# Kernel tuning notes

Measured on AMD Instinct MI355X. Metric: run time of the kernel, lower is better.

## Reference

```python
import jax, jax.numpy as jnp
import numpy as np

N_EMBED = 1024
NUM_EXPERTS = 8
TOP_K = 2
N_ROUTERS = 5
SEQ = 2048


def setup_inputs() -> dict:
    key = jax.random.key(0)
    ks = jax.random.split(key, 10)
    d, E, R, H = N_EMBED, NUM_EXPERTS, N_ROUTERS, 4 * N_EMBED
    x = jax.random.normal(ks[0], (R, SEQ, d), dtype=jnp.float32)
    moe = jnp.arange(R, dtype=jnp.int64) if jax.config.jax_enable_x64 else jnp.arange(R, dtype=jnp.int32)
    s = 0.02
    Wr = s * jax.random.normal(ks[1], (R, d, E), dtype=jnp.float32)
    br = jnp.zeros((R, E), dtype=jnp.float32)
    Wn = s * jax.random.normal(ks[2], (R, d, E), dtype=jnp.float32)
    bn = jnp.zeros((R, E), dtype=jnp.float32)
    W1 = s * jax.random.normal(ks[3], (E, d, H), dtype=jnp.float32)
    b1 = jnp.zeros((E, H), dtype=jnp.float32)
    W2 = s * jax.random.normal(ks[4], (E, H, d), dtype=jnp.float32)
    b2 = jnp.zeros((E, d), dtype=jnp.float32)
    return {"x": x, "moe": moe, "Wr": Wr, "br": br, "Wn": Wn, "bn": bn,
            "W1": W1, "b1": b1, "W2": W2, "b2": b2}


def reference(x, moe, Wr, br, Wn, bn, W1, b1, W2, b2):
    # Per-batch router selection: router[moe[b]] applied to x[b]
    logits = jnp.einsum('btd,bde->bte', x, Wr[moe]) + br[moe][:, None, :]
    noise_logits = jnp.einsum('btd,bde->bte', x, Wn[moe]) + bn[moe][:, None, :]
    eps = jax.random.normal(jax.random.key(42), logits.shape, logits.dtype)
    noisy = logits + eps * jax.nn.softplus(noise_logits)  # [B,T,E]

    topv, topi = jax.lax.top_k(noisy, TOP_K)  # [B,T,K]
    E = noisy.shape[-1]
    # selected[b,t,e] = e in top-k indices; equivalent to scatter of top-k logits into -inf
    selected = jnp.any(topi[..., None] == jnp.arange(E), axis=-2)  # [B,T,E]
    sparse = jnp.where(selected, noisy, -jnp.inf)
    gating = jax.nn.softmax(sparse, axis=-1)  # zero for non-selected experts

    B, T, d = x.shape
    flat_x = x.reshape(-1, d)            # [B*T, d]
    flat_g = gating.reshape(-1, E)       # [B*T, E]
    out = jnp.zeros_like(flat_x)
    for e in range(E):  # fixed small set of experts
        h = jax.nn.relu(flat_x @ W1[e] + b1[e])   # [B*T, 4d]
        o = h @ W2[e] + b2[e]                      # [B*T, d]
        out = out + o * flat_g[:, e:e + 1]         # gating is 0 off top-k
    final_output = out.reshape(B, T, d)
    return final_output, topi
```

## Files before the change

### kernel.cpp

```cpp
#include <hip/hip_runtime.h>
#include <hip/hip_bf16.h>
#include <cstdint>

#define NTOK   10240
#define DIM    1024
#define NEXP   8
#define HDIM   4096
#define NSLOT  20480
#define MAXSLOT 21504
#define MAXTILES 168

typedef __attribute__((ext_vector_type(8))) __bf16 bf16x8;
typedef __attribute__((ext_vector_type(4))) float  f32x4;

__device__ __forceinline__ unsigned short f2bf(float f){
  uint32_t u = __float_as_uint(f);
  uint32_t r = (u + 0x7fffu + ((u >> 16) & 1u)) >> 16;
  return (unsigned short)r;
}
__device__ __forceinline__ float bf2f(unsigned short u){
  return __uint_as_float(((uint32_t)u) << 16);
}

__device__ __forceinline__ void gl_lds16(const void* g, void* l){
  __builtin_amdgcn_global_load_lds(
      (const __attribute__((address_space(1))) void*)g,
      (__attribute__((address_space(3))) void*)l, 16, 0, 0);
}

__device__ __forceinline__ int swz_wid(){
  int nwg = (int)(gridDim.x * gridDim.y);
  int h   = (int)(blockIdx.y * gridDim.x + blockIdx.x);
  int q = nwg >> 3, r = nwg & 7;
  int xcd = h & 7, idx = h >> 3;
  return (xcd < r ? xcd*(q+1) : r*(q+1) + (xcd-r)*q) + idx;
}

__device__ __forceinline__ uint32_t rotl32(uint32_t x, int n){ return (x << n) | (x >> (32 - n)); }

__device__ __forceinline__ uint32_t threefry_xor(uint32_t k0, uint32_t k1, uint32_t x0, uint32_t x1){
  uint32_t ks2 = k0 ^ k1 ^ 0x1BD11BDAu;
  uint32_t ks[3] = {k0, k1, ks2};
  x0 += ks[0]; x1 += ks[1];
  const int rA[4] = {13,15,26,6};
  const int rB[4] = {17,29,16,24};
  #pragma unroll
  for (int i = 0; i < 5; ++i){
    #pragma unroll
    for (int j = 0; j < 4; ++j){
      int rot = (i & 1) ? rB[j] : rA[j];
      x0 += x1; x1 = rotl32(x1, rot); x1 ^= x0;
    }
    x0 += ks[(i+1)%3];
    x1 += ks[(i+2)%3] + (uint32_t)(i+1);
  }
  return x0 ^ x1;
}

__device__ __forceinline__ float erfinv_f32(float x){
  float w = -log1pf(-x*x);
  float p;
  if (w < 5.0f){
    w -= 2.5f;
    p = 2.81022636e-08f;
    p = fmaf(p, w, 3.43273939e-07f);
    p = fmaf(p, w, -3.5233877e-06f);
    p = fmaf(p, w, -4.39150654e-06f);
    p = fmaf(p, w, 0.00021858087f);
    p = fmaf(p, w, -0.00125372503f);
    p = fmaf(p, w, -0.00417768164f);
    p = fmaf(p, w, 0.246640727f);
    p = fmaf(p, w, 1.50140941f);
  } else {
    w = sqrtf(w) - 3.0f;
    p = -0.000200214257f;
    p = fmaf(p, w, 0.000100950558f);
    p = fmaf(p, w, 0.00134934322f);
    p = fmaf(p, w, -0.00367342844f);
    p = fmaf(p, w, 0.00573950773f);
    p = fmaf(p, w, -0.0076224613f);
    p = fmaf(p, w, 0.00943887047f);
    p = fmaf(p, w, 1.00167406f);
    p = fmaf(p, w, 2.83297682f);
  }
  return p * x;
}

__global__ void transpose_cvt_kernel(const float* __restrict__ src, unsigned short* __restrict__ dst,
                                     int R_, int C_){
  __shared__ float tile[32][33];
  int z = blockIdx.z;
  const float* s = src + (size_t)z * R_ * C_;
  unsigned short* d = dst + (size_t)z * R_ * C_;
  int c0 = blockIdx.x * 32, r0 = blockIdx.y * 32;
  #pragma unroll
  for (int i = threadIdx.y; i < 32; i += 8)
    tile[i][threadIdx.x] = s[(size_t)(r0 + i) * C_ + c0 + threadIdx.x];
  __syncthreads();
  #pragma unroll
  for (int i = threadIdx.y; i < 32; i += 8)
    d[(size_t)(c0 + i) * R_ + r0 + threadIdx.x] = f2bf(tile[threadIdx.x][i]);
}

__global__ __launch_bounds__(256) void route_kernel(
    const float* __restrict__ x, const int* __restrict__ moe,
    const float* __restrict__ Wr, const float* __restrict__ br,
    const float* __restrict__ Wn, const float* __restrict__ bn,
    float* __restrict__ topi_out, int* __restrict__ te, float* __restrict__ tgv,
    unsigned short* __restrict__ xb)
{
  const int wv = threadIdx.x >> 6, lane = threadIdx.x & 63;
  const int tok = (int)blockIdx.x * 4 + wv;
  const int b = tok >> 11;
  const int r = moe[b];
  const float4* xr  = (const float4*)(x + (size_t)tok * DIM);
  const float4* wrp = (const float4*)(Wr + (size_t)r * DIM * NEXP);
  const float4* wnp = (const float4*)(Wn + (size_t)r * DIM * NEXP);
  ushort4* xbrow = (ushort4*)(xb + (size_t)tok * DIM);

  float lg[8], nl[8];
  #pragma unroll
  for (int e = 0; e < 8; ++e){ lg[e] = 0.f; nl[e] = 0.f; }

  #pragma unroll
  for (int it = 0; it < 4; ++it){
    int d4 = it*64 + lane;
    float4 xv = xr[d4];
    ushort4 o;
    o.x = f2bf(xv.x); o.y = f2bf(xv.y); o.z = f2bf(xv.z); o.w = f2bf(xv.w);
    xbrow[d4] = o;
    #pragma unroll
    for (int j = 0; j < 4; ++j){
      float xs = (j==0) ? xv.x : (j==1) ? xv.y : (j==2) ? xv.z : xv.w;
      float4 w0 = wrp[d4*8 + j*2], w1 = wrp[d4*8 + j*2 + 1];
      float4 n0 = wnp[d4*8 + j*2], n1 = wnp[d4*8 + j*2 + 1];
      lg[0] = fmaf(xs, w0.x, lg[0]); lg[1] = fmaf(xs, w0.y, lg[1]);
      lg[2] = fmaf(xs, w0.z, lg[2]); lg[3] = fmaf(xs, w0.w, lg[3]);
      lg[4] = fmaf(xs, w1.x, lg[4]); lg[5] = fmaf(xs, w1.y, lg[5]);
      lg[6] = fmaf(xs, w1.z, lg[6]); lg[7] = fmaf(xs, w1.w, lg[7]);
      nl[0] = fmaf(xs, n0.x, nl[0]); nl[1] = fmaf(xs, n0.y, nl[1]);
      nl[2] = fmaf(xs, n0.z, nl[2]); nl[3] = fmaf(xs, n0.w, nl[3]);
      nl[4] = fmaf(xs, n1.x, nl[4]); nl[5] = fmaf(xs, n1.y, nl[5]);
      nl[6] = fmaf(xs, n1.z, nl[6]); nl[7] = fmaf(xs, n1.w, nl[7]);
    }
  }

  #pragma unroll
  for (int e = 0; e < 8; ++e){
    #pragma unroll
    for (int s = 32; s >= 1; s >>= 1){
      lg[e] += __shfl_xor(lg[e], s, 64);
      nl[e] += __shfl_xor(nl[e], s, 64);
    }
  }

  int el = lane & 7;
  float mylg = lg[0], mynl = nl[0];
  #pragma unroll
  for (int e = 1; e < 8; ++e){
    if (el == e){ mylg = lg[e]; mynl = nl[e]; }
  }
  float logit = mylg + br[r*NEXP + el];
  float nlg   = mynl + bn[r*NEXP + el];
  uint32_t idx  = (uint32_t)(tok*NEXP + el);
  uint32_t bits = threefry_xor(0u, 42u, 0u, idx);
  float u01 = __uint_as_float((bits >> 9) | 0x3f800000u) - 1.0f;
  const float lo = -0.99999994f;
  float uu  = fmaxf(lo, u01 * 2.0f + lo);
  float eps = 1.41421356237f * erfinv_f32(uu);
  float ax = fabsf(nlg);
  float sp = fmaxf(nlg, 0.0f) + log1pf(expf(-ax));
  float noisy = logit + eps * sp;

  float nv[8];
  #pragma unroll
  for (int e = 0; e < 8; ++e) nv[e] = __shfl(noisy, e, 64);

  if (lane == 0){
    int i0 = 0; float v0 = nv[0];
    int i1 = -1; float v1 = -3.4e38f;
    #pragma unroll
    for (int e = 1; e < 8; ++e){
      float v = nv[e];
      if (v > v0){ v1 = v0; i1 = i0; v0 = v; i0 = e; }
      else if (v > v1){ v1 = v; i1 = e; }
    }
    float t = expf(v1 - v0);
    float s = 1.0f + t;
    topi_out[tok*2 + 0] = (float)i0;
    topi_out[tok*2 + 1] = (float)i1;
    te[tok*2 + 0] = i0; te[tok*2 + 1] = i1;
    tgv[tok*2 + 0] = 1.0f / s; tgv[tok*2 + 1] = t / s;
  }
}

__global__ __launch_bounds__(256) void count_kernel(const int* __restrict__ te,
                                                    unsigned* __restrict__ counts){
  int id = blockIdx.x * 256 + threadIdx.x;
  int e = te[id];
  int lane = threadIdx.x & 63;
  #pragma unroll
  for (int ee = 0; ee < 8; ++ee){
    unsigned long long m = __ballot(e == ee);
    if (m && lane == (__ffsll((unsigned long long)m) - 1))
      atomicAdd(&counts[ee], (unsigned)__popcll(m));
  }
}

__global__ void tables_kernel(unsigned* __restrict__ hdr, int* __restrict__ tile_expert,
                              int* __restrict__ rows)
{
  __shared__ unsigned offs_s[NEXP+1];
  __shared__ unsigned cnt_s[NEXP];
  if (threadIdx.x == 0){
    unsigned o = 0, tt = 0;
    for (int e = 0; e < NEXP; ++e){
      unsigned c = hdr[e];
      cnt_s[e] = c;
      offs_s[e] = o;
      hdr[8 + e] = o;
      unsigned nt = (c + 127u) / 128u;
      for (unsigned k = 0; k < nt; ++k) tile_expert[tt++] = e;
      o += nt * 128u;
    }
    offs_s[NEXP] = o;
    hdr[16] = tt;
  }
  __syncthreads();
  for (int e = 0; e < NEXP; ++e){
    unsigned start = offs_s[e] + cnt_s[e];
    unsigned end   = offs_s[e+1];
    for (unsigned i = start + threadIdx.x; i < end; i += blockDim.x)
      rows[i] = 0;
  }
}

__global__ __launch_bounds__(256) void scatter_kernel(const int* __restrict__ te,
                               unsigned* __restrict__ cursor, int* __restrict__ rows,
                               int* __restrict__ slot_idx)
{
  int id = blockIdx.x * 256 + threadIdx.x;
  int tok = id >> 1;
  int e = te[id];
  int lane = threadIdx.x & 63;
  unsigned long long below = ((unsigned long long)1 << lane) - 1ull;
  unsigned myslot = 0;
  #pragma unroll
  for (int ee = 0; ee < 8; ++ee){
    unsigned long long m = __ballot(e == ee);
    if (e == ee){
      int leader = __ffsll((unsigned long long)m) - 1;
      unsigned base = 0;
      if (lane == leader) base = atomicAdd(&cursor[ee], (unsigned)__popcll(m));
      base = __shfl(base, leader, 64);
      myslot = base + (unsigned)__popcll(m & below);
    }
  }
  rows[myslot] = tok;
  slot_idx[id] = (int)myslot;
}

__global__ __launch_bounds__(512) void gemm1_kernel(
    const unsigned short* __restrict__ Xb,
    const unsigned short* __restrict__ W1t,
    const float* __restrict__ b1,
    const int* __restrict__ rows, const int* __restrict__ tile_expert,
    const unsigned* __restrict__ hdr,
    unsigned short* __restrict__ H)
{
  const int w  = swz_wid();
  const int xn = w % (int)gridDim.x;
  const int tg = w / (int)gridDim.x;
  if (tg >= (int)hdr[16]) return;
  const int e  = tile_expert[tg];
  const int n0 = xn * 128;
  const int tid = threadIdx.x;
  const int wid = tid >> 6, lane = tid & 63;
  const int wr = wid >> 2, wc = wid & 3;
  const int l8 = lane & 7, ld8 = lane >> 3;
  const int srcsw = (l8 ^ ld8) * 8;
  const int l15 = lane & 15, lq = lane >> 4, l7 = lane & 7;

  __shared__ __align__(16) unsigned short As[2][128][64];
  __shared__ __align__(16) unsigned short Bs[2][128][64];

  const unsigned short* aSrc[2];
  const unsigned short* bSrc[2];
  #pragma unroll
  for (int i = 0; i < 2; ++i){
    int rrow = wid*16 + i*8 + ld8;
    int tokr = rows[tg*128 + rrow];
    aSrc[i] = Xb  + (size_t)tokr * DIM + srcsw;
    bSrc[i] = W1t + ((size_t)e * HDIM + n0 + rrow) * DIM + srcsw;
  }

  f32x4 acc[4][2];
  #pragma unroll
  for (int m = 0; m < 4; ++m)
    #pragma unroll
    for (int n = 0; n < 2; ++n) acc[m][n] = (f32x4)(0.0f);

  auto stage = [&](int b, int kk){
    #pragma unroll
    for (int i = 0; i < 2; ++i){
      gl_lds16(aSrc[i] + kk, &As[b][wid*16 + i*8][0]);
      gl_lds16(bSrc[i] + kk, &Bs[b][wid*16 + i*8][0]);
    }
  };

  stage(0, 0);
  __builtin_amdgcn_sched_barrier(0);

  const int NT = DIM / 64;
  int cur = 0;
  for (int t = 0; t < NT; ++t){
    if (t + 1 < NT){
      stage(cur ^ 1, (t + 1) * 64);
      __builtin_amdgcn_sched_barrier(0);
      asm volatile("s_waitcnt vmcnt(4)" ::: "memory");
    } else {
      asm volatile("s_waitcnt vmcnt(0)" ::: "memory");
    }
    __builtin_amdgcn_sched_barrier(0);
    __builtin_amdgcn_s_barrier();
    __builtin_amdgcn_sched_barrier(0);

    #pragma unroll
    for (int ks = 0; ks < 2; ++ks){
      const int ch = ((ks*4 + lq) ^ l7) * 8;
      bf16x8 af[4], bfv[2];
      #pragma unroll
      for (int m = 0; m < 4; ++m)
        af[m] = *reinterpret_cast<const bf16x8*>(&As[cur][wr*64 + m*16 + l15][ch]);
      #pragma unroll
      for (int n = 0; n < 2; ++n)
        bfv[n] = *reinterpret_cast<const bf16x8*>(&Bs[cur][wc*32 + n*16 + l15][ch]);
      __builtin_amdgcn_s_setprio(1);
      #pragma unroll
      for (int m = 0; m < 4; ++m)
        #pragma unroll
        for (int n = 0; n < 2; ++n)
          acc[m][n] = __builtin_amdgcn_mfma_f32_16x16x32_bf16(af[m], bfv[n], acc[m][n], 0, 0, 0);
      __builtin_amdgcn_s_setprio(0);
    }
    __builtin_amdgcn_sched_barrier(0);
    __builtin_amdgcn_s_barrier();
    __builtin_amdgcn_sched_barrier(0);
    cur ^= 1;
  }

  const int hrow0 = tg * 128;
  #pragma unroll
  for (int n = 0; n < 2; ++n){
    int c = n0 + wc*32 + n*16 + l15;
    float bv = b1[(size_t)e * HDIM + c];
    #pragma unroll
    for (int m = 0; m < 4; ++m){
      #pragma unroll
      for (int j = 0; j < 4; ++j){
        int rloc = wr*64 + m*16 + lq*4 + j;
        float v = fmaxf(acc[m][n][j] + bv, 0.0f);
        H[(size_t)(hrow0 + rloc) * HDIM + c] = f2bf(v);
      }
    }
  }
}

__global__ __launch_bounds__(512) void gemm2_kernel(
    const unsigned short* __restrict__ H,
    const unsigned short* __restrict__ W2t,
    const float* __restrict__ b2,
    const int* __restrict__ tile_expert, const unsigned* __restrict__ hdr,
    unsigned short* __restrict__ O2)
{
  const int w  = swz_wid();
  const int xn = w % (int)gridDim.x;
  const int tg = w / (int)gridDim.x;
  if (tg >= (int)hdr[16]) return;
  const int e  = tile_expert[tg];
  const int n0 = xn * 128;
  const int tid = threadIdx.x;
  const int wid = tid >> 6, lane = tid & 63;
  const int wr = wid >> 2, wc = wid & 3;
  const int l8 = lane & 7, ld8 = lane >> 3;
  const int srcsw = (l8 ^ ld8) * 8;
  const int l15 = lane & 15, lq = lane >> 4, l7 = lane & 7;

  __shared__ __align__(16) unsigned short As[2][128][64];
  __shared__ __align__(16) unsigned short Bs[2][128][64];

  const unsigned short* aSrc[2];
  const unsigned short* bSrc[2];
  #pragma unroll
  for (int i = 0; i < 2; ++i){
    int rrow = wid*16 + i*8 + ld8;
    aSrc[i] = H   + (size_t)(tg*128 + rrow) * HDIM + srcsw;
    bSrc[i] = W2t + ((size_t)e * DIM + n0 + rrow) * HDIM + srcsw;
  }

  f32x4 acc[4][2];
  #pragma unroll
  for (int m = 0; m < 4; ++m)
    #pragma unroll
    for (int n = 0; n < 2; ++n) acc[m][n] = (f32x4)(0.0f);

  auto stage = [&](int b, int kk){
    #pragma unroll
    for (int i = 0; i < 2; ++i){
      gl_lds16(aSrc[i] + kk, &As[b][wid*16 + i*8][0]);
      gl_lds16(bSrc[i] + kk, &Bs[b][wid*16 + i*8][0]);
    }
  };

  stage(0, 0);
  __builtin_amdgcn_sched_barrier(0);

  const int NT = HDIM / 64;
  int cur = 0;
  for (int t = 0; t < NT; ++t){
    if (t + 1 < NT){
      stage(cur ^ 1, (t + 1) * 64);
      __builtin_amdgcn_sched_barrier(0);
      asm volatile("s_waitcnt vmcnt(4)" ::: "memory");
    } else {
      asm volatile("s_waitcnt vmcnt(0)" ::: "memory");
    }
    __builtin_amdgcn_sched_barrier(0);
    __builtin_amdgcn_s_barrier();
    __builtin_amdgcn_sched_barrier(0);

    #pragma unroll
    for (int ks = 0; ks < 2; ++ks){
      const int ch = ((ks*4 + lq) ^ l7) * 8;
      bf16x8 af[4], bfv[2];
      #pragma unroll
      for (int m = 0; m < 4; ++m)
        af[m] = *reinterpret_cast<const bf16x8*>(&As[cur][wr*64 + m*16 + l15][ch]);
      #pragma unroll
      for (int n = 0; n < 2; ++n)
        bfv[n] = *reinterpret_cast<const bf16x8*>(&Bs[cur][wc*32 + n*16 + l15][ch]);
      __builtin_amdgcn_s_setprio(1);
      #pragma unroll
      for (int m = 0; m < 4; ++m)
        #pragma unroll
        for (int n = 0; n < 2; ++n)
          acc[m][n] = __builtin_amdgcn_mfma_f32_16x16x32_bf16(af[m], bfv[n], acc[m][n], 0, 0, 0);
      __builtin_amdgcn_s_setprio(0);
    }
    __builtin_amdgcn_sched_barrier(0);
    __builtin_amdgcn_s_barrier();
    __builtin_amdgcn_sched_barrier(0);
    cur ^= 1;
  }

  #pragma unroll
  for (int n = 0; n < 2; ++n){
    int c = n0 + wc*32 + n*16 + l15;
    float bv = b2[(size_t)e * DIM + c];
    #pragma unroll
    for (int m = 0; m < 4; ++m){
      #pragma unroll
      for (int j = 0; j < 4; ++j){
        int rloc = wr*64 + m*16 + lq*4 + j;
        O2[(size_t)(tg*128 + rloc) * DIM + c] = f2bf(acc[m][n][j] + bv);
      }
    }
  }
}

__global__ __launch_bounds__(256) void combine_kernel(
    const unsigned short* __restrict__ O2, const int* __restrict__ slot_idx,
    const float* __restrict__ tgv, float* __restrict__ out)
{
  int tok = blockIdx.x;
  int d4  = threadIdx.x;
  int s0 = slot_idx[tok*2], s1 = slot_idx[tok*2 + 1];
  float g0 = tgv[tok*2], g1 = tgv[tok*2 + 1];
  ushort4 a = ((const ushort4*)(O2 + (size_t)s0 * DIM))[d4];
  ushort4 b = ((const ushort4*)(O2 + (size_t)s1 * DIM))[d4];
  float4 o;
  o.x = g0*bf2f(a.x) + g1*bf2f(b.x);
  o.y = g0*bf2f(a.y) + g1*bf2f(b.y);
  o.z = g0*bf2f(a.z) + g1*bf2f(b.z);
  o.w = g0*bf2f(a.w) + g1*bf2f(b.w);
  ((float4*)(out + (size_t)tok * DIM))[d4] = o;
}

extern "C" void kernel_launch(void* const* d_in, const int* in_sizes, int n_in,
                              void* d_out, int out_size, void* d_ws, size_t ws_size,
                              hipStream_t stream)
{
  const float* x  = (const float*)d_in[0];
  const int*   moe= (const int*)  d_in[1];
  const float* Wr = (const float*)d_in[2];
  const float* br = (const float*)d_in[3];
  const float* Wn = (const float*)d_in[4];
  const float* bn = (const float*)d_in[5];
  const float* W1 = (const float*)d_in[6];
  const float* b1 = (const float*)d_in[7];
  const float* W2 = (const float*)d_in[8];
  const float* b2 = (const float*)d_in[9];
  float* out = (float*)d_out;
  float* topi_out = out + (size_t)NTOK * DIM;

  char* ws = (char*)d_ws;
  size_t off = 0;
  auto take = [&](size_t bytes)->char*{
    char* p = ws + off;
    off = (off + bytes + 255) & ~(size_t)255;
    return p;
  };
  unsigned* hdr        = (unsigned*)take(128);
  int*      tile_exp   = (int*)     take(MAXTILES * 4);
  int*      rows       = (int*)     take(MAXSLOT * 4);
  int*      te         = (int*)     take(NSLOT * 4);
  float*    tgv        = (float*)   take(NSLOT * 4);
  int*      slot_idx   = (int*)     take(NSLOT * 4);
  unsigned short* xb   = (unsigned short*)take((size_t)NTOK * DIM * 2);
  unsigned short* W1t  = (unsigned short*)take((size_t)NEXP * HDIM * DIM * 2);
  unsigned short* W2t  = (unsigned short*)take((size_t)NEXP * DIM * HDIM * 2);
  unsigned short* O2   = (unsigned short*)take((size_t)MAXSLOT * DIM * 2);

  size_t avail = (ws_size > off) ? (ws_size - off) : 0;
  size_t maxrows = avail / ((size_t)HDIM * 2);
  int tpc = (int)(maxrows / 128);
  if (tpc > MAXTILES) tpc = MAXTILES;
  if (tpc < 1) tpc = 1;
  unsigned short* H = (unsigned short*)take((size_t)tpc * 128 * HDIM * 2);

  hipMemsetAsync(hdr, 0, 128, stream);

  dim3 tb(32, 8);
  transpose_cvt_kernel<<<dim3(HDIM/32, DIM/32, NEXP), tb, 0, stream>>>(W1, W1t, DIM, HDIM);
  transpose_cvt_kernel<<<dim3(DIM/32, HDIM/32, NEXP), tb, 0, stream>>>(W2, W2t, HDIM, DIM);
  route_kernel<<<NTOK/4, 256, 0, stream>>>(x, moe, Wr, br, Wn, bn, topi_out, te, tgv, xb);
  count_kernel<<<NSLOT/256, 256, 0, stream>>>(te, hdr);
  tables_kernel<<<1, 64, 0, stream>>>(hdr, tile_exp, rows);
  scatter_kernel<<<NSLOT/256, 256, 0, stream>>>(te, hdr + 8, rows, slot_idx);

  if (tpc >= MAXTILES){
    gemm1_kernel<<<dim3(HDIM/128, MAXTILES), 512, 0, stream>>>(xb, W1t, b1, rows, tile_exp, hdr, H);
    gemm2_kernel<<<dim3(DIM/128,  MAXTILES), 512, 0, stream>>>(H, W2t, b2, tile_exp, hdr, O2);
  } else {
    for (int t0 = 0; t0 < MAXTILES; t0 += tpc){
      int nt = (tpc < MAXTILES - t0) ? tpc : (MAXTILES - t0);
      unsigned short* Hoff = H - (size_t)t0 * 128 * HDIM;
      gemm1_kernel<<<dim3(HDIM/128, nt), 512, 0, stream>>>(xb, W1t, b1, rows + t0*128,
                                                           tile_exp + t0, hdr, Hoff);
      gemm2_kernel<<<dim3(DIM/128,  nt), 512, 0, stream>>>(Hoff, W2t, b2, tile_exp + t0, hdr,
                                                           O2 + (size_t)t0*128*DIM);
    }
  }
  combine_kernel<<<NTOK, 256, 0, stream>>>(O2, slot_idx, tgv, out);
}
```

Before: 735.5 us.

## Merge weight transposes into routing kernel and deepen GEMM prefetch pipeline

Folds the two weight transpose/convert launches into the routing kernel as extra blocks, saving launches and letting the transposes overlap with routing. Both expert GEMMs switch from a 2-stage pipeline over 64-wide K slices to a 4-slot pipeline over 32-wide half-tiles with three stages in flight, which hides more global-load latency. The XOR swizzle on LDS is dropped in favour of a plain 32-column layout. That may add LDS bank conflicts, and it doubles the barriers per unit of K.

```diff
diff --git a/kernel.cpp b/kernel.cpp
--- a/kernel.cpp
+++ b/kernel.cpp
@@ -86,33 +86,49 @@
   return p * x;
 }
 
-__global__ void transpose_cvt_kernel(const float* __restrict__ src, unsigned short* __restrict__ dst,
-                                     int R_, int C_){
+__device__ __forceinline__ void transpose_body(const float* __restrict__ src,
+                                               unsigned short* __restrict__ dst,
+                                               int R_, int C_, int bx, int by, int z){
   __shared__ float tile[32][33];
-  int z = blockIdx.z;
+  const int tx = threadIdx.x & 31, ty = threadIdx.x >> 5;
   const float* s = src + (size_t)z * R_ * C_;
   unsigned short* d = dst + (size_t)z * R_ * C_;
-  int c0 = blockIdx.x * 32, r0 = blockIdx.y * 32;
-  #pragma unroll
-  for (int i = threadIdx.y; i < 32; i += 8)
-    tile[i][threadIdx.x] = s[(size_t)(r0 + i) * C_ + c0 + threadIdx.x];
+  int c0 = bx * 32, r0 = by * 32;
+  #pragma unroll
+  for (int i = ty; i < 32; i += 8)
+    tile[i][tx] = s[(size_t)(r0 + i) * C_ + c0 + tx];
   __syncthreads();
   #pragma unroll
-  for (int i = threadIdx.y; i < 32; i += 8)
-    d[(size_t)(c0 + i) * R_ + r0 + threadIdx.x] = f2bf(tile[threadIdx.x][i]);
-}
-
-__global__ __launch_bounds__(256) void route_kernel(
+  for (int i = ty; i < 32; i += 8)
+    d[(size_t)(c0 + i) * R_ + r0 + tx] = f2bf(tile[tx][i]);
+}
+
+__global__ __launch_bounds__(256) void prep_kernel(
     const float* __restrict__ x, const int* __restrict__ moe,
     const float* __restrict__ Wr, const float* __restrict__ br,
     const float* __restrict__ Wn, const float* __restrict__ bn,
+    const float* __restrict__ W1, const float* __restrict__ W2,
     float* __restrict__ topi_out, int* __restrict__ te, float* __restrict__ tgv,
-    unsigned short* __restrict__ xb)
-{
+    unsigned short* __restrict__ xb,
+    unsigned short* __restrict__ W1t, unsigned short* __restrict__ W2t)
+{
+  const int b = (int)blockIdx.x;
+  const int NROUTE = NTOK/4;
+  if (b >= NROUTE){
+    int i = b - NROUTE;
+    if (i < 32768){
+      transpose_body(W1, W1t, DIM, HDIM, i & 127, (i >> 7) & 31, i >> 12);
+    } else {
+      i -= 32768;
+      transpose_body(W2, W2t, HDIM, DIM, i & 31, (i >> 5) & 127, i >> 12);
+    }
+    return;
+  }
+
   const int wv = threadIdx.x >> 6, lane = threadIdx.x & 63;
-  const int tok = (int)blockIdx.x * 4 + wv;
-  const int b = tok >> 11;
-  const int r = moe[b];
+  const int tok = b * 4 + wv;
+  const int bb = tok >> 11;
+  const int r = moe[bb];
   const float4* xr  = (const float4*)(x + (size_t)tok * DIM);
   const float4* wrp = (const float4*)(Wr + (size_t)r * DIM * NEXP);
   const float4* wnp = (const float4*)(Wn + (size_t)r * DIM * NEXP);
@@ -277,22 +293,16 @@
   const int tid = threadIdx.x;
   const int wid = tid >> 6, lane = tid & 63;
   const int wr = wid >> 2, wc = wid & 3;
-  const int l8 = lane & 7, ld8 = lane >> 3;
-  const int srcsw = (l8 ^ ld8) * 8;
-  const int l15 = lane & 15, lq = lane >> 4, l7 = lane & 7;
-
-  __shared__ __align__(16) unsigned short As[2][128][64];
-  __shared__ __align__(16) unsigned short Bs[2][128][64];
-
-  const unsigned short* aSrc[2];
-  const unsigned short* bSrc[2];
-  #pragma unroll
-  for (int i = 0; i < 2; ++i){
-    int rrow = wid*16 + i*8 + ld8;
-    int tokr = rows[tg*128 + rrow];
-    aSrc[i] = Xb  + (size_t)tokr * DIM + srcsw;
-    bSrc[i] = W1t + ((size_t)e * HDIM + n0 + rrow) * DIM + srcsw;
-  }
+  const int l15 = lane & 15, lq = lane >> 4;
+  const int srow = wid*16 + (lane >> 2);
+  const int sch  = lane & 3;
+
+  __shared__ __align__(16) unsigned short As[2][2][128][32];
+  __shared__ __align__(16) unsigned short Bs[2][2][128][32];
+
+  const int tokr = rows[tg*128 + srow];
+  const unsigned short* aRow = Xb  + (size_t)tokr * DIM + sch*8;
+  const unsigned short* bRow = W1t + ((size_t)e * HDIM + n0 + srow) * DIM + sch*8;
 
   f32x4 acc[4][2];
   #pragma unroll
@@ -300,53 +310,45 @@
     #pragma unroll
     for (int n = 0; n < 2; ++n) acc[m][n] = (f32x4)(0.0f);
 
-  auto stage = [&](int b, int kk){
-    #pragma unroll
-    for (int i = 0; i < 2; ++i){
-      gl_lds16(aSrc[i] + kk, &As[b][wid*16 + i*8][0]);
-      gl_lds16(bSrc[i] + kk, &Bs[b][wid*16 + i*8][0]);
-    }
+  auto stage = [&](int h){
+    gl_lds16(aRow + h*32, &As[(h>>1)&1][h&1][wid*16][0]);
+    gl_lds16(bRow + h*32, &Bs[(h>>1)&1][h&1][wid*16][0]);
   };
 
-  stage(0, 0);
+  const int HT = DIM / 32;
+  stage(0); stage(1); stage(2);
   __builtin_amdgcn_sched_barrier(0);
 
-  const int NT = DIM / 64;
-  int cur = 0;
-  for (int t = 0; t < NT; ++t){
-    if (t + 1 < NT){
-      stage(cur ^ 1, (t + 1) * 64);
-      __builtin_amdgcn_sched_barrier(0);
-      asm volatile("s_waitcnt vmcnt(4)" ::: "memory");
-    } else {
-      asm volatile("s_waitcnt vmcnt(0)" ::: "memory");
-    }
+  for (int h = 0; h < HT; ++h){
+    if (h + 3 < HT) stage(h + 3);
+    __builtin_amdgcn_sched_barrier(0);
+    int rem = HT - 1 - h;
+    if (rem >= 3)      asm volatile("s_waitcnt vmcnt(6)" ::: "memory");
+    else if (rem == 2) asm volatile("s_waitcnt vmcnt(4)" ::: "memory");
+    else if (rem == 1) asm volatile("s_waitcnt vmcnt(2)" ::: "memory");
+    else               asm volatile("s_waitcnt vmcnt(0)" ::: "memory");
     __builtin_amdgcn_sched_barrier(0);
     __builtin_amdgcn_s_barrier();
     __builtin_amdgcn_sched_barrier(0);
 
-    #pragma unroll
-    for (int ks = 0; ks < 2; ++ks){
-      const int ch = ((ks*4 + lq) ^ l7) * 8;
-      bf16x8 af[4], bfv[2];
-      #pragma unroll
-      for (int m = 0; m < 4; ++m)
-        af[m] = *reinterpret_cast<const bf16x8*>(&As[cur][wr*64 + m*16 + l15][ch]);
+    const int bsel = (h >> 1) & 1, hsel = h & 1;
+    bf16x8 af[4], bfv[2];
+    #pragma unroll
+    for (int m = 0; m < 4; ++m)
+      af[m] = *reinterpret_cast<const bf16x8*>(&As[bsel][hsel][wr*64 + m*16 + l15][lq*8]);
+    #pragma unroll
+    for (int n = 0; n < 2; ++n)
+      bfv[n] = *reinterpret_cast<const bf16x8*>(&Bs[bsel][hsel][wc*32 + n*16 + l15][lq*8]);
+    __builtin_amdgcn_s_setprio(1);
+    #pragma unroll
+    for (int m = 0; m < 4; ++m)
       #pragma unroll
       for (int n = 0; n < 2; ++n)
-        bfv[n] = *reinterpret_cast<const bf16x8*>(&Bs[cur][wc*32 + n*16 + l15][ch]);
-      __builtin_amdgcn_s_setprio(1);
-      #pragma unroll
-      for (int m = 0; m < 4; ++m)
-        #pragma unroll
-        for (int n = 0; n < 2; ++n)
-          acc[m][n] = __builtin_amdgcn_mfma_f32_16x16x32_bf16(af[m], bfv[n], acc[m][n], 0, 0, 0);
-      __builtin_amdgcn_s_setprio(0);
-    }
+        acc[m][n] = __builtin_amdgcn_mfma_f32_16x16x32_bf16(af[m], bfv[n], acc[m][n], 0, 0, 0);
+    __builtin_amdgcn_s_setprio(0);
     __builtin_amdgcn_sched_barrier(0);
     __builtin_amdgcn_s_barrier();
     __builtin_amdgcn_sched_barrier(0);
-    cur ^= 1;
   }
 
   const int hrow0 = tg * 128;
@@ -382,21 +384,15 @@
   const int tid = threadIdx.x;
   const int wid = tid >> 6, lane = tid & 63;
   const int wr = wid >> 2, wc = wid & 3;
-  const int l8 = lane & 7, ld8 = lane >> 3;
-  const int srcsw = (l8 ^ ld8) * 8;
-  const int l15 = lane & 15, lq = lane >> 4, l7 = lane & 7;
-
-  __shared__ __align__(16) unsigned short As[2][128][64];
-  __shared__ __align__(16) unsigned short Bs[2][128][64];
-
-  const unsigned short* aSrc[2];
-  const unsigned short* bSrc[2];
-  #pragma unroll
-  for (int i = 0; i < 2; ++i){
-    int rrow = wid*16 + i*8 + ld8;
-    aSrc[i] = H   + (size_t)(tg*128 + rrow) * HDIM + srcsw;
-    bSrc[i] = W2t + ((size_t)e * DIM + n0 + rrow) * HDIM + srcsw;
-  }
+  const int l15 = lane & 15, lq = lane >> 4;
+  const int srow = wid*16 + (lane >> 2);
+  const int sch  = lane & 3;
+
+  __shared__ __align__(16) unsigned short As[2][2][128][32];
+  __shared__ __align__(16) unsigned short Bs[2][2][128][32];
+
+  const unsigned short* aRow = H   + (size_t)(tg*128 + srow) * HDIM + sch*8;
+  const unsigned short* bRow = W2t + ((size_t)e * DIM + n0 + srow) * HDIM + sch*8;
 
   f32x4 acc[4][2];
   #pragma unroll
@@ -404,53 +400,45 @@
     #pragma unroll
     for (int n = 0; n < 2; ++n) acc[m][n] = (f32x4)(0.0f);
 
-  auto stage = [&](int b, int kk){
-    #pragma unroll
-    for (int i = 0; i < 2; ++i){
-      gl_lds16(aSrc[i] + kk, &As[b][wid*16 + i*8][0]);
-      gl_lds16(bSrc[i] + kk, &Bs[b][wid*16 + i*8][0]);
-    }
+  auto stage = [&](int h){
+    gl_lds16(aRow + h*32, &As[(h>>1)&1][h&1][wid*16][0]);
+    gl_lds16(bRow + h*32, &Bs[(h>>1)&1][h&1][wid*16][0]);
   };
 
-  stage(0, 0);
+  const int HT = HDIM / 32;
+  stage(0); stage(1); stage(2);
   __builtin_amdgcn_sched_barrier(0);
 
-  const int NT = HDIM / 64;
-  int cur = 0;
-  for (int t = 0; t < NT; ++t){
-    if (t + 1 < NT){
-      stage(cur ^ 1, (t + 1) * 64);
-      __builtin_amdgcn_sched_barrier(0);
-      asm volatile("s_waitcnt vmcnt(4)" ::: "memory");
-    } else {
-      asm volatile("s_waitcnt vmcnt(0)" ::: "memory");
-    }
+  for (int h = 0; h < HT; ++h){
+    if (h + 3 < HT) stage(h + 3);
+    __builtin_amdgcn_sched_barrier(0);
+    int rem = HT - 1 - h;
+    if (rem >= 3)      asm volatile("s_waitcnt vmcnt(6)" ::: "memory");
+    else if (rem == 2) asm volatile("s_waitcnt vmcnt(4)" ::: "memory");
+    else if (rem == 1) asm volatile("s_waitcnt vmcnt(2)" ::: "memory");
+    else               asm volatile("s_waitcnt vmcnt(0)" ::: "memory");
     __builtin_amdgcn_sched_barrier(0);
     __builtin_amdgcn_s_barrier();
     __builtin_amdgcn_sched_barrier(0);
 
-    #pragma unroll
-    for (int ks = 0; ks < 2; ++ks){
-      const int ch = ((ks*4 + lq) ^ l7) * 8;
-      bf16x8 af[4], bfv[2];
-      #pragma unroll
-      for (int m = 0; m < 4; ++m)
-        af[m] = *reinterpret_cast<const bf16x8*>(&As[cur][wr*64 + m*16 + l15][ch]);
+    const int bsel = (h >> 1) & 1, hsel = h & 1;
+    bf16x8 af[4], bfv[2];
+    #pragma unroll
+    for (int m = 0; m < 4; ++m)
+      af[m] = *reinterpret_cast<const bf16x8*>(&As[bsel][hsel][wr*64 + m*16 + l15][lq*8]);
+    #pragma unroll
+    for (int n = 0; n < 2; ++n)
+      bfv[n] = *reinterpret_cast<const bf16x8*>(&Bs[bsel][hsel][wc*32 + n*16 + l15][lq*8]);
+    __builtin_amdgcn_s_setprio(1);
+    #pragma unroll
+    for (int m = 0; m < 4; ++m)
       #pragma unroll
       for (int n = 0; n < 2; ++n)
-        bfv[n] = *reinterpret_cast<const bf16x8*>(&Bs[cur][wc*32 + n*16 + l15][ch]);
-      __builtin_amdgcn_s_setprio(1);
-      #pragma unroll
-      for (int m = 0; m < 4; ++m)
-        #pragma unroll
-        for (int n = 0; n < 2; ++n)
-          acc[m][n] = __builtin_amdgcn_mfma_f32_16x16x32_bf16(af[m], bfv[n], acc[m][n], 0, 0, 0);
-      __builtin_amdgcn_s_setprio(0);
-    }
+        acc[m][n] = __builtin_amdgcn_mfma_f32_16x16x32_bf16(af[m], bfv[n], acc[m][n], 0, 0, 0);
+    __builtin_amdgcn_s_setprio(0);
     __builtin_amdgcn_sched_barrier(0);
     __builtin_amdgcn_s_barrier();
     __builtin_amdgcn_sched_barrier(0);
-    cur ^= 1;
   }
 
   #pragma unroll
@@ -530,10 +518,8 @@
 
   hipMemsetAsync(hdr, 0, 128, stream);
 
-  dim3 tb(32, 8);
-  transpose_cvt_kernel<<<dim3(HDIM/32, DIM/32, NEXP), tb, 0, stream>>>(W1, W1t, DIM, HDIM);
-  transpose_cvt_kernel<<<dim3(DIM/32, HDIM/32, NEXP), tb, 0, stream>>>(W2, W2t, HDIM, DIM);
-  route_kernel<<<NTOK/4, 256, 0, stream>>>(x, moe, Wr, br, Wn, bn, topi_out, te, tgv, xb);
+  prep_kernel<<<NTOK/4 + 65536, 256, 0, stream>>>(x, moe, Wr, br, Wn, bn, W1, W2,
+                                                  topi_out, te, tgv, xb, W1t, W2t);
   count_kernel<<<NSLOT/256, 256, 0, stream>>>(te, hdr);
   tables_kernel<<<1, 64, 0, stream>>>(hdr, tile_exp, rows);
   scatter_kernel<<<NSLOT/256, 256, 0, stream>>>(te, hdr + 8, rows, slot_idx);
```

After: 870.6 us. +18.4%, slower.
